# Kernel optimization log

Measured on AMD Instinct MI355X. Metric: run time of the kernel, lower is better.

## Reference

```python
import jax, jax.numpy as jnp
import numpy as np

B = 32      # batch
N = 1024    # input_size (= maxval)
EPS = 1.0   # regularization_strength


def _isotonic_l2(y):
    """Non-increasing isotonic regression (L2) of each row of y: [B, n].

    Uses the minimax characterization  sol_i = min_{j<=i} max_{k>=i} mean(y[j..k]),
    which equals the PAV solution and yields the correct block-averaging Jacobian
    under autodiff. O(n^2) memory per row, fully vectorized.
    """
    b, n = y.shape
    cs = jnp.concatenate([jnp.zeros((b, 1), y.dtype), jnp.cumsum(y, axis=-1)], axis=-1)  # [B, n+1]
    j = jnp.arange(n)[:, None]   # start index
    k = jnp.arange(n)[None, :]   # end index
    length = (k - j + 1).astype(y.dtype)
    # M[b, j, k] = mean(y[b, j..k]) for k >= j
    M = (cs[:, None, 1:] - cs[:, :-1, None]) / jnp.where(k >= j, length, jnp.ones_like(length))
    M = jnp.where(k >= j, M, -jnp.inf)
    # Amax[b, j, i] = max_{k >= i} M[b, j, k]  (suffix max along k)
    Amax = jax.lax.cummax(M, axis=2, reverse=True)
    # restrict to j <= i, then minimize over j
    Amax = jnp.where(j <= k, Amax, jnp.inf)  # here the k-axis plays the role of i
    return jnp.min(Amax, axis=1)  # [B, n]


def _soft_rank(x, eps):
    """fast-soft-sort soft_rank, direction=ASCENDING, regularization='l2'."""
    b, n = x.shape
    theta = x / eps
    perm = jnp.argsort(-theta, axis=-1)                 # descending sort permutation
    s = jnp.take_along_axis(theta, perm, axis=-1)       # sorted (descending)
    w = jnp.arange(n, 0, -1, dtype=x.dtype)             # [n, n-1, ..., 1]
    sol = _isotonic_l2(s - w)                           # dual solution
    primal = s - sol                                    # projection, sorted order
    inv = jnp.argsort(perm, axis=-1)
    return jnp.take_along_axis(primal, inv, axis=-1)    # unpermute -> ranks in [1, n]


def setup_inputs() -> dict:
    key = jax.random.key(0)
    x = jax.random.normal(key, (B, N), dtype=jnp.float32)
    return {"x": x}


def reference(x) -> jnp.ndarray:
    ranks = _soft_rank(x, EPS)                          # [B, n]
    n = x.shape[1]
    t = jnp.arange(1, n + 1, dtype=x.dtype)             # rank targets 1..n
    # out[b, j, i] = relu(1 - |ranks[b, j] - (i + 1)|)  (== torch .permute(0, 2, 1) result)
    return jax.nn.relu(1.0 - jnp.abs(ranks[:, :, None] - t[None, None, :]))
```

## Files before the change

### kernel.cpp

```cpp
#include <hip/hip_runtime.h>
#include <stdint.h>

#define N 1024
#define BATCH 32

__global__ __launch_bounds__(256) void count_kernel(const float* __restrict__ x,
                                                    int* __restrict__ pos_g) {
    __shared__ uint64_t keys[N];
    __shared__ int      partial[256];

    const int row   = blockIdx.x >> 4;
    const int chunk = blockIdx.x & 15;
    const int t     = threadIdx.x;

    const float4 xq = reinterpret_cast<const float4*>(x + row * N)[t];
    {
        const float vv[4] = {xq.x, xq.y, xq.z, xq.w};
        const int j0 = t << 2;
        #pragma unroll
        for (int e = 0; e < 4; ++e) {
            uint32_t u = __float_as_uint(vv[e]);
            u ^= (u & 0x80000000u) ? 0xFFFFFFFFu : 0x80000000u;
            keys[j0 + e] = (((uint64_t)u) << 10) | (uint64_t)(1023 - (j0 + e));
        }
    }
    __syncthreads();

    const int e = (chunk << 6) + (t & 63);
    const int q = t >> 6;
    const uint64_t kk = keys[e];
    const int kbeg = q << 8;
    int c = 0;
    #pragma unroll 4
    for (int k = kbeg; k < kbeg + 256; k += 4) {
        c += (int)(keys[k    ] > kk);
        c += (int)(keys[k + 1] > kk);
        c += (int)(keys[k + 2] > kk);
        c += (int)(keys[k + 3] > kk);
    }
    partial[t] = c;
    __syncthreads();

    if (t < 64)
        pos_g[row * N + e] = partial[t] + partial[t + 64] + partial[t + 128] + partial[t + 192];
}

__global__ __launch_bounds__(256) void ranks_kernel(const float* __restrict__ x,
                                                    const int* __restrict__ pos_g,
                                                    float* __restrict__ ranks) {
    __shared__ float    ss[N];
    __shared__ float    yv[N];
    __shared__ double   csum[N];
    __shared__ int      segid[N];
    __shared__ int      run_start[N+1];
    __shared__ float    run_mean[N];
    __shared__ double   stk_sum[N];
    __shared__ int      stk_cnt[N];
    __shared__ int      stk_runs[N];
    __shared__ double   wsumD[4];
    __shared__ int      wsumI[4];

    const int b = blockIdx.x;
    const int t = threadIdx.x;
    const int j0 = t << 2;
    const int lane = t & 63;
    const int wid = t >> 6;

    const float4 xq = reinterpret_cast<const float4*>(x + b * N)[t];
    const int4   pq = reinterpret_cast<const int4*>(pos_g + b * N)[t];
    ss[pq.x] = xq.x; ss[pq.y] = xq.y; ss[pq.z] = xq.z; ss[pq.w] = xq.w;
    __syncthreads();

    float4 yq;
    {
        const float4 sq = reinterpret_cast<const float4*>(ss)[t];
        yq.x = sq.x + (float)(j0 - 512);
        yq.y = sq.y + (float)(j0 - 511);
        yq.z = sq.z + (float)(j0 - 510);
        yq.w = sq.w + (float)(j0 - 509);
        reinterpret_cast<float4*>(yv)[t] = yq;
    }
    __syncthreads();

    const float ye[4] = {yq.x, yq.y, yq.z, yq.w};
    int    fl[4];
    int    lf[4];
    double lys[4];
    {
        float prev = (j0 == 0) ? -1.0e30f : yv[j0 - 1];
        double accy = 0.0; int accf = 0;
        #pragma unroll
        for (int e = 0; e < 4; ++e) {
            const int f = (prev > ye[e]) ? 1 : 0;
            prev = ye[e];
            fl[e] = f;
            accf += f;             lf[e]  = accf;
            accy += (double)ye[e]; lys[e] = accy;
        }
    }
    double vy = lys[3]; int vf = lf[3];
    #pragma unroll
    for (int off = 1; off < 64; off <<= 1) {
        const double oy = __shfl_up(vy, off);
        const int    of = __shfl_up(vf, off);
        if (lane >= off) { vy += oy; vf += of; }
    }
    if (lane == 63) { wsumD[wid] = vy; wsumI[wid] = vf; }
    __syncthreads();
    {
        double basey = vy - lys[3]; int basef = vf - lf[3];
        for (int w = 0; w < wid; ++w) { basey += wsumD[w]; basef += wsumI[w]; }
        #pragma unroll
        for (int e = 0; e < 4; ++e) {
            const int p   = j0 + e;
            const int seg = basef + lf[e];
            segid[p] = seg;
            csum[p]  = basey + lys[e];
            if (fl[e]) run_start[seg] = p;
        }
        if (t == 0) run_start[0] = 0;
    }
    __syncthreads();

    if (t == 0) {
        const int R = segid[N - 1] + 1;
        run_start[R] = N;
        int sp = 0;
        for (int r = 0; r < R; ++r) {
            const int a   = run_start[r];
            const int bnd = run_start[r + 1];
            double s = csum[bnd - 1] - ((a > 0) ? csum[a - 1] : 0.0);
            int    c = bnd - a;
            int    nr = 1;
            while (sp > 0 && s * (double)stk_cnt[sp - 1] > stk_sum[sp - 1] * (double)c) {
                s  += stk_sum[sp - 1];
                c  += stk_cnt[sp - 1];
                nr += stk_runs[sp - 1];
                --sp;
            }
            stk_sum[sp] = s; stk_cnt[sp] = c; stk_runs[sp] = nr; ++sp;
        }
        int rc = 0;
        for (int e2 = 0; e2 < sp; ++e2) {
            const float m = (float)(stk_sum[e2] / (double)stk_cnt[e2]);
            for (int q2 = 0; q2 < stk_runs[e2]; ++q2) run_mean[rc++] = m;
        }
    }
    __syncthreads();

    float4 r4;
    r4.x = xq.x - run_mean[segid[pq.x]] + 512.0f;
    r4.y = xq.y - run_mean[segid[pq.y]] + 512.0f;
    r4.z = xq.z - run_mean[segid[pq.z]] + 512.0f;
    r4.w = xq.w - run_mean[segid[pq.w]] + 512.0f;
    reinterpret_cast<float4*>(ranks + b * N)[t] = r4;
}

__global__ __launch_bounds__(256) void fill_kernel(const float* __restrict__ ranks,
                                                   float* __restrict__ out) {
    const int r0 = blockIdx.x << 2;
    const int i = threadIdx.x << 2;
    const float ra = ranks[r0 + 0];
    const float rb = ranks[r0 + 1];
    const float rc = ranks[r0 + 2];
    const float rd = ranks[r0 + 3];
    const float rv[4] = {ra, rb, rc, rd};
    #pragma unroll
    for (int rr = 0; rr < 4; ++rr) {
        const float r = rv[rr];
        float4 o;
        o.x = fmaxf(1.0f - fabsf(r - (float)(i + 1)), 0.0f);
        o.y = fmaxf(1.0f - fabsf(r - (float)(i + 2)), 0.0f);
        o.z = fmaxf(1.0f - fabsf(r - (float)(i + 3)), 0.0f);
        o.w = fmaxf(1.0f - fabsf(r - (float)(i + 4)), 0.0f);
        reinterpret_cast<float4*>(out + (size_t)(r0 + rr) * N)[threadIdx.x] = o;
    }
}

extern "C" void kernel_launch(void* const* d_in, const int* in_sizes, int n_in,
                              void* d_out, int out_size, void* d_ws, size_t ws_size,
                              hipStream_t stream) {
    const float* x = (const float*)d_in[0];
    float* out = (float*)d_out;
    int*   pos_g = (int*)d_ws;
    float* ranks = (float*)d_ws + BATCH * N;

    count_kernel<<<BATCH * 16, 256, 0, stream>>>(x, pos_g);
    ranks_kernel<<<BATCH, 256, 0, stream>>>(x, pos_g, ranks);
    fill_kernel<<<(BATCH * N) / 4, 256, 0, stream>>>(ranks, out);
}
```

Baseline: 140.3 us.

## Fuse count, ranks and fill kernels into one cooperative kernel with grid sync

Replaces the three kernel launches with a single cooperative kernel of 256 blocks that runs the counting-sort position pass, the per-row PAV isotonic pass and the output fill. Phases are separated by grid.sync(). The goal is to remove launch overhead and inter-kernel gaps. In exchange it uses fewer blocks for the fill and count phases, leaves most blocks idle during the serial PAV phase, pays the cost of two grid barriers, and needs enough shared memory per block for all phases. If the cooperative launch fails, it falls back to the original three kernels.

```diff
diff --git a/kernel.cpp b/kernel.cpp
--- a/kernel.cpp
+++ b/kernel.cpp
@@ -1,8 +1,193 @@
 #include <hip/hip_runtime.h>
+#include <hip/hip_cooperative_groups.h>
 #include <stdint.h>
+
+namespace cg = cooperative_groups;
 
 #define N 1024
 #define BATCH 32
+#define GRID 256
+
+__global__ __launch_bounds__(256) void fused_kernel(const float* __restrict__ x,
+                                                    int* __restrict__ pos_g,
+                                                    float* __restrict__ ranks,
+                                                    float* __restrict__ out) {
+    __shared__ uint64_t keys[N];
+    __shared__ int      partial[256];
+    __shared__ float    ss[N];
+    __shared__ float    yv[N];
+    __shared__ double   csum[N];
+    __shared__ int      segid[N];
+    __shared__ int      run_start[N+1];
+    __shared__ float    run_mean[N];
+    __shared__ double   stk_sum[N];
+    __shared__ int      stk_cnt[N];
+    __shared__ int      stk_runs[N];
+    __shared__ double   wsumD[4];
+    __shared__ int      wsumI[4];
+
+    cg::grid_group grid = cg::this_grid();
+    const int t = threadIdx.x;
+
+    {
+        const int row   = blockIdx.x >> 3;
+        const int chunk = blockIdx.x & 7;
+
+        const float4 xq = reinterpret_cast<const float4*>(x + row * N)[t];
+        {
+            const float vv[4] = {xq.x, xq.y, xq.z, xq.w};
+            const int j0 = t << 2;
+            #pragma unroll
+            for (int e = 0; e < 4; ++e) {
+                uint32_t u = __float_as_uint(vv[e]);
+                u ^= (u & 0x80000000u) ? 0xFFFFFFFFu : 0x80000000u;
+                keys[j0 + e] = (((uint64_t)u) << 10) | (uint64_t)(1023 - (j0 + e));
+            }
+        }
+        __syncthreads();
+
+        const int e    = (chunk << 7) + (t & 127);
+        const int half = t >> 7;
+        const uint64_t kk = keys[e];
+        const int kbeg = half << 9;
+        int c = 0;
+        #pragma unroll 4
+        for (int k = kbeg; k < kbeg + 512; k += 4) {
+            c += (int)(keys[k    ] > kk);
+            c += (int)(keys[k + 1] > kk);
+            c += (int)(keys[k + 2] > kk);
+            c += (int)(keys[k + 3] > kk);
+        }
+        partial[t] = c;
+        __syncthreads();
+
+        if (t < 128) pos_g[row * N + e] = partial[t] + partial[t + 128];
+    }
+
+    grid.sync();
+
+    if (blockIdx.x < BATCH) {
+        const int b = blockIdx.x;
+        const int j0 = t << 2;
+        const int lane = t & 63;
+        const int wid = t >> 6;
+
+        const float4 xq = reinterpret_cast<const float4*>(x + b * N)[t];
+        const int4   pq = reinterpret_cast<const int4*>(pos_g + b * N)[t];
+        ss[pq.x] = xq.x; ss[pq.y] = xq.y; ss[pq.z] = xq.z; ss[pq.w] = xq.w;
+        __syncthreads();
+
+        float4 yq;
+        {
+            const float4 sq = reinterpret_cast<const float4*>(ss)[t];
+            yq.x = sq.x + (float)(j0 - 512);
+            yq.y = sq.y + (float)(j0 - 511);
+            yq.z = sq.z + (float)(j0 - 510);
+            yq.w = sq.w + (float)(j0 - 509);
+            reinterpret_cast<float4*>(yv)[t] = yq;
+        }
+        __syncthreads();
+
+        const float ye[4] = {yq.x, yq.y, yq.z, yq.w};
+        int    fl[4];
+        int    lf[4];
+        double lys[4];
+        {
+            float prev = (j0 == 0) ? -1.0e30f : yv[j0 - 1];
+            double accy = 0.0; int accf = 0;
+            #pragma unroll
+            for (int e = 0; e < 4; ++e) {
+                const int f = (prev > ye[e]) ? 1 : 0;
+                prev = ye[e];
+                fl[e] = f;
+                accf += f;             lf[e]  = accf;
+                accy += (double)ye[e]; lys[e] = accy;
+            }
+        }
+        double vy = lys[3]; int vf = lf[3];
+        #pragma unroll
+        for (int off = 1; off < 64; off <<= 1) {
+            const double oy = __shfl_up(vy, off);
+            const int    of = __shfl_up(vf, off);
+            if (lane >= off) { vy += oy; vf += of; }
+        }
+        if (lane == 63) { wsumD[wid] = vy; wsumI[wid] = vf; }
+        __syncthreads();
+        {
+            double basey = vy - lys[3]; int basef = vf - lf[3];
+            for (int w = 0; w < wid; ++w) { basey += wsumD[w]; basef += wsumI[w]; }
+            #pragma unroll
+            for (int e = 0; e < 4; ++e) {
+                const int p   = j0 + e;
+                const int seg = basef + lf[e];
+                segid[p] = seg;
+                csum[p]  = basey + lys[e];
+                if (fl[e]) run_start[seg] = p;
+            }
+            if (t == 0) run_start[0] = 0;
+        }
+        __syncthreads();
+
+        if (t == 0) {
+            const int R = segid[N - 1] + 1;
+            run_start[R] = N;
+            int sp = 0;
+            for (int r = 0; r < R; ++r) {
+                const int a   = run_start[r];
+                const int bnd = run_start[r + 1];
+                double s = csum[bnd - 1] - ((a > 0) ? csum[a - 1] : 0.0);
+                int    c = bnd - a;
+                int    nr = 1;
+                while (sp > 0 && s * (double)stk_cnt[sp - 1] > stk_sum[sp - 1] * (double)c) {
+                    s  += stk_sum[sp - 1];
+                    c  += stk_cnt[sp - 1];
+                    nr += stk_runs[sp - 1];
+                    --sp;
+                }
+                stk_sum[sp] = s; stk_cnt[sp] = c; stk_runs[sp] = nr; ++sp;
+            }
+            int rc = 0;
+            for (int e2 = 0; e2 < sp; ++e2) {
+                const float m = (float)(stk_sum[e2] / (double)stk_cnt[e2]);
+                for (int q2 = 0; q2 < stk_runs[e2]; ++q2) run_mean[rc++] = m;
+            }
+        }
+        __syncthreads();
+
+        float4 r4;
+        r4.x = xq.x - run_mean[segid[pq.x]] + 512.0f;
+        r4.y = xq.y - run_mean[segid[pq.y]] + 512.0f;
+        r4.z = xq.z - run_mean[segid[pq.z]] + 512.0f;
+        r4.w = xq.w - run_mean[segid[pq.w]] + 512.0f;
+        reinterpret_cast<float4*>(ranks + b * N)[t] = r4;
+    }
+
+    grid.sync();
+
+    {
+        const int i = t << 2;
+        const int base_row = blockIdx.x << 7;
+        #pragma unroll 4
+        for (int g = 0; g < 32; ++g) {
+            const int r0 = base_row + (g << 2);
+            const float ra = ranks[r0 + 0];
+            const float rb = ranks[r0 + 1];
+            const float rc = ranks[r0 + 2];
+            const float rd = ranks[r0 + 3];
+            const float rv[4] = {ra, rb, rc, rd};
+            #pragma unroll
+            for (int rr = 0; rr < 4; ++rr) {
+                const float r = rv[rr];
+                float4 o;
+                o.x = fmaxf(1.0f - fabsf(r - (float)(i + 1)), 0.0f);
+                o.y = fmaxf(1.0f - fabsf(r - (float)(i + 2)), 0.0f);
+                o.z = fmaxf(1.0f - fabsf(r - (float)(i + 3)), 0.0f);
+                o.w = fmaxf(1.0f - fabsf(r - (float)(i + 4)), 0.0f);
+                reinterpret_cast<float4*>(out + (size_t)(r0 + rr) * N)[t] = o;
+            }
+        }
+    }
+}
 
 __global__ __launch_bounds__(256) void count_kernel(const float* __restrict__ x,
                                                     int* __restrict__ pos_g) {
@@ -185,7 +370,13 @@
     int*   pos_g = (int*)d_ws;
     float* ranks = (float*)d_ws + BATCH * N;
 
-    count_kernel<<<BATCH * 16, 256, 0, stream>>>(x, pos_g);
-    ranks_kernel<<<BATCH, 256, 0, stream>>>(x, pos_g, ranks);
-    fill_kernel<<<(BATCH * N) / 4, 256, 0, stream>>>(ranks, out);
-}
+    void* kargs[] = {(void*)&x, (void*)&pos_g, (void*)&ranks, (void*)&out};
+    hipError_t err = hipLaunchCooperativeKernel((const void*)fused_kernel,
+                                                dim3(GRID), dim3(256),
+                                                kargs, 0, stream);
+    if (err != hipSuccess) {
+        count_kernel<<<BATCH * 16, 256, 0, stream>>>(x, pos_g);
+        ranks_kernel<<<BATCH, 256, 0, stream>>>(x, pos_g, ranks);
+        fill_kernel<<<(BATCH * N) / 4, 256, 0, stream>>>(ranks, out);
+    }
+}
```

New measurement: 220.5 us. 57.1% more time.
